# Optimization experiments

Measured on AMD Instinct MI355X. Metric: run time of the kernel, lower is better.

Reference implementation:

```python
import jax, jax.numpy as jnp
import numpy as np

N_LAYERS = 3
NUM_NODES = 400000
EMB_DIM = 64
N_EDGES = 4000000


def setup_inputs() -> dict:
    key = jax.random.key(0)
    k1, k2, k3, k4 = jax.random.split(key, 4)
    embedding = jax.random.normal(k1, (NUM_NODES, EMB_DIM), dtype=jnp.float32) * 0.1
    adj_row = jax.random.randint(k2, (N_EDGES,), 0, NUM_NODES, dtype=jnp.int64)
    adj_col = jax.random.randint(k3, (N_EDGES,), 0, NUM_NODES, dtype=jnp.int64)
    # normalized adjacency values (e.g. 1/sqrt(d_i d_j)); positive, small
    adj_val = jax.random.uniform(k4, (N_EDGES,), dtype=jnp.float32) * 0.01
    return {"embedding": embedding, "adj_row": adj_row, "adj_col": adj_col, "adj_val": adj_val}


def _spmm(row, col, val, x):
    # sparse [N,N] @ dense [N,D]: gather neighbor rows, scale, scatter-add
    msgs = val[:, None] * x[col]                      # [E, D]
    return jax.ops.segment_sum(msgs, row, num_segments=NUM_NODES)


def reference(embedding, adj_row, adj_col, adj_val):
    # LightGCN propagation: running mean over layer outputs (fused accumulator,
    # mathematically identical to stack+mean over n_layers+1 embeddings)
    x = embedding
    acc = x
    for _ in range(N_LAYERS):
        x = _spmm(adj_row, adj_col, adj_val, x)
        acc = acc + x
    all_embeddings = acc / jnp.asarray(N_LAYERS + 1, dtype=x.dtype)
    return all_embeddings
```

## Files before the change

kernel.cpp:

```cpp
#include <hip/hip_runtime.h>

#define EMB 64
#define SCAN_B 256
#define RPB 32
#define RPW 8
#define ECAP 1024

typedef unsigned uint2v __attribute__((ext_vector_type(2)));
typedef float float4v __attribute__((ext_vector_type(4)));

__device__ inline uint2 nt_load_u2(const uint2* p) {
    uint2v v = __builtin_nontemporal_load((const uint2v*)p);
    return make_uint2(v.x, v.y);
}
__device__ inline void nt_store_u2(uint2* p, uint2 v) {
    uint2v t; t.x = v.x; t.y = v.y;
    __builtin_nontemporal_store(t, (uint2v*)p);
}
__device__ inline float4 nt_load_f4(const float4* p) {
    float4v v = __builtin_nontemporal_load((const float4v*)p);
    return make_float4(v.x, v.y, v.z, v.w);
}
__device__ inline void nt_store_f4(float4* p, float4 v) {
    float4v t; t.x = v.x; t.y = v.y; t.z = v.z; t.w = v.w;
    __builtin_nontemporal_store(t, (float4v*)p);
}

__device__ inline unsigned short f2bf(float f) {
    unsigned u = __float_as_uint(f);
    return (unsigned short)((u + 0x7fffu + ((u >> 16) & 1u)) >> 16);
}
__device__ inline float bl(unsigned u) { return __uint_as_float(u << 16); }
__device__ inline float bh(unsigned u) { return __uint_as_float(u & 0xffff0000u); }


__global__ void zero_ints(int* __restrict__ p, int n) {
    int i = blockIdx.x * blockDim.x + threadIdx.x;
    if (i < n) p[i] = 0;
}

__global__ void hist_rows(const int* __restrict__ row, int* __restrict__ S, int E) {
    int e = blockIdx.x * blockDim.x + threadIdx.x;
    if (e < E) atomicAdd(&S[__builtin_nontemporal_load(row + e)], 1);
}

__global__ void scan_block_sums(const int* __restrict__ S, int* __restrict__ bsum, int N) {
    __shared__ int sdata[SCAN_B];
    int i = blockIdx.x * SCAN_B + threadIdx.x;
    sdata[threadIdx.x] = (i < N) ? S[i] : 0;
    __syncthreads();
    for (int off = SCAN_B / 2; off > 0; off >>= 1) {
        if (threadIdx.x < off) sdata[threadIdx.x] += sdata[threadIdx.x + off];
        __syncthreads();
    }
    if (threadIdx.x == 0) bsum[blockIdx.x] = sdata[0];
}

__global__ void scan_sums(int* __restrict__ bsum, int nb) {
    __shared__ int part[1024];
    int t = threadIdx.x;
    int i0 = 2 * t, i1 = 2 * t + 1;
    int a = (i0 < nb) ? bsum[i0] : 0;
    int b = (i1 < nb) ? bsum[i1] : 0;
    part[t] = a + b;
    __syncthreads();
    for (int off = 1; off < 1024; off <<= 1) {
        int v = part[t];
        int add = (t >= off) ? part[t - off] : 0;
        __syncthreads();
        part[t] = v + add;
        __syncthreads();
    }
    int excl = (t == 0) ? 0 : part[t - 1];
    if (i0 < nb) bsum[i0] = excl;
    if (i1 < nb) bsum[i1] = excl + a;
}

__global__ void scan_apply(int* __restrict__ S, const int* __restrict__ bsum, int N) {
    __shared__ int sdata[SCAN_B];
    int i = blockIdx.x * SCAN_B + threadIdx.x;
    int v = (i < N) ? S[i] : 0;
    sdata[threadIdx.x] = v;
    __syncthreads();
    for (int off = 1; off < SCAN_B; off <<= 1) {
        int val = sdata[threadIdx.x];
        int add = (threadIdx.x >= off) ? sdata[threadIdx.x - off] : 0;
        __syncthreads();
        sdata[threadIdx.x] = val + add;
        __syncthreads();
    }
    int excl = (threadIdx.x == 0 ? 0 : sdata[threadIdx.x - 1]) + bsum[blockIdx.x];
    if (i < N) S[i] = excl;
}

__global__ void scatter_edges_ranged(const int* __restrict__ row, const int* __restrict__ col,
                                     const float* __restrict__ val,
                                     int* __restrict__ S, uint2* __restrict__ epack,
                                     int E, int rstep) {
    int pass  = blockIdx.x & 7;
    int chunk = blockIdx.x >> 3;
    int e = chunk * blockDim.x + threadIdx.x;
    if (e >= E) return;
    int r = __builtin_nontemporal_load(row + e);
    int lo = pass * rstep;
    if (r < lo || r >= lo + rstep) return;
    int c = __builtin_nontemporal_load(col + e);
    float v = __builtin_nontemporal_load(val + e);
    int pos = atomicAdd(&S[r], 1);
    epack[pos] = make_uint2((unsigned)c, __float_as_uint(v));
}

__global__ void conv_bf16(const float4* __restrict__ src, uint2* __restrict__ dst, int n4) {
    int i = blockIdx.x * blockDim.x + threadIdx.x;
    if (i < n4) {
        float4 v = nt_load_f4(src + i);
        unsigned w0 = (unsigned)f2bf(v.x) | ((unsigned)f2bf(v.y) << 16);
        unsigned w1 = (unsigned)f2bf(v.z) | ((unsigned)f2bf(v.w) << 16);
        nt_store_u2(dst + i, make_uint2(w0, w1));
    }
}

template<bool STG>
__device__ __forceinline__ void spmm_rows(
    const uint2* __restrict__ epack, const uint2* __restrict__ esh, int beg0,
    const int* __restrict__ Ssh, int j0,
    const unsigned short* __restrict__ x, const float* __restrict__ emb,
    unsigned short* __restrict__ y, float* __restrict__ acc,
    int rb, int N, int mode, int lane, int grp, int d4)
{
    const uint2 z2 = make_uint2(0u, 0u);

#define EDG(i) (STG ? esh[(i) - beg0] : epack[i])
#define LOADR(J, B_, E_, P0, P1, P2, P3, G0, G1, G2, G3)                         \
    {                                                                            \
        B_ = Ssh[J]; E_ = Ssh[(J) + 1];                                          \
        int i0 = B_ + grp, i1 = i0 + 4, i2 = i0 + 8, i3 = i0 + 12;               \
        P0 = (i0 < E_) ? EDG(i0) : z2;                                           \
        P1 = (i1 < E_) ? EDG(i1) : z2;                                           \
        P2 = (i2 < E_) ? EDG(i2) : z2;                                           \
        P3 = (i3 < E_) ? EDG(i3) : z2;                                           \
        G0 = (i0 < E_) ? ((const uint2*)(x + ((size_t)P0.x << 6)))[d4] : z2;     \
        G1 = (i1 < E_) ? ((const uint2*)(x + ((size_t)P1.x << 6)))[d4] : z2;     \
        G2 = (i2 < E_) ? ((const uint2*)(x + ((size_t)P2.x << 6)))[d4] : z2;     \
        G3 = (i3 < E_) ? ((const uint2*)(x + ((size_t)P3.x << 6)))[d4] : z2;     \
    }

    int aB = 0, aE = 0;
    uint2 ap0 = z2, ap1 = z2, ap2 = z2, ap3 = z2, ag0 = z2, ag1 = z2, ag2 = z2, ag3 = z2;
    int bB = 0, bE = 0;
    uint2 bp0 = z2, bp1 = z2, bp2 = z2, bp3 = z2, bg0 = z2, bg1 = z2, bg2 = z2, bg3 = z2;

    LOADR(j0, aB, aE, ap0, ap1, ap2, ap3, ag0, ag1, ag2, ag3);

    for (int k = 0; k < RPW; ++k) {
        int j = j0 + k;
        int r = rb + j;
        if (k + 1 < RPW) {
            LOADR(j + 1, bB, bE, bp0, bp1, bp2, bp3, bg0, bg1, bg2, bg3);
        }

        float4 s = make_float4(0.f, 0.f, 0.f, 0.f);
        {
            int i0 = aB + grp, i1 = i0 + 4, i2 = i0 + 8, i3 = i0 + 12;
            float w0 = (i0 < aE) ? __uint_as_float(ap0.y) : 0.f;
            float w1 = (i1 < aE) ? __uint_as_float(ap1.y) : 0.f;
            float w2 = (i2 < aE) ? __uint_as_float(ap2.y) : 0.f;
            float w3 = (i3 < aE) ? __uint_as_float(ap3.y) : 0.f;
            s.x += w0 * bl(ag0.x); s.y += w0 * bh(ag0.x); s.z += w0 * bl(ag0.y); s.w += w0 * bh(ag0.y);
            s.x += w1 * bl(ag1.x); s.y += w1 * bh(ag1.x); s.z += w1 * bl(ag1.y); s.w += w1 * bh(ag1.y);
            s.x += w2 * bl(ag2.x); s.y += w2 * bh(ag2.x); s.z += w2 * bl(ag2.y); s.w += w2 * bh(ag2.y);
            s.x += w3 * bl(ag3.x); s.y += w3 * bh(ag3.x); s.z += w3 * bl(ag3.y); s.w += w3 * bh(ag3.y);
        }
        for (int base = aB + 16; base < aE; base += 16) {
            int i0 = base + grp, i1 = i0 + 4, i2 = i0 + 8, i3 = i0 + 12;
            uint2 p0 = (i0 < aE) ? EDG(i0) : z2;
            uint2 p1 = (i1 < aE) ? EDG(i1) : z2;
            uint2 p2 = (i2 < aE) ? EDG(i2) : z2;
            uint2 p3 = (i3 < aE) ? EDG(i3) : z2;
            uint2 g0 = (i0 < aE) ? ((const uint2*)(x + ((size_t)p0.x << 6)))[d4] : z2;
            uint2 g1 = (i1 < aE) ? ((const uint2*)(x + ((size_t)p1.x << 6)))[d4] : z2;
            uint2 g2 = (i2 < aE) ? ((const uint2*)(x + ((size_t)p2.x << 6)))[d4] : z2;
            uint2 g3 = (i3 < aE) ? ((const uint2*)(x + ((size_t)p3.x << 6)))[d4] : z2;
            float w0 = (i0 < aE) ? __uint_as_float(p0.y) : 0.f;
            float w1 = (i1 < aE) ? __uint_as_float(p1.y) : 0.f;
            float w2 = (i2 < aE) ? __uint_as_float(p2.y) : 0.f;
            float w3 = (i3 < aE) ? __uint_as_float(p3.y) : 0.f;
            s.x += w0 * bl(g0.x); s.y += w0 * bh(g0.x); s.z += w0 * bl(g0.y); s.w += w0 * bh(g0.y);
            s.x += w1 * bl(g1.x); s.y += w1 * bh(g1.x); s.z += w1 * bl(g1.y); s.w += w1 * bh(g1.y);
            s.x += w2 * bl(g2.x); s.y += w2 * bh(g2.x); s.z += w2 * bl(g2.y); s.w += w2 * bh(g2.y);
            s.x += w3 * bl(g3.x); s.y += w3 * bh(g3.x); s.z += w3 * bl(g3.y); s.w += w3 * bh(g3.y);
        }

        s.x += __shfl_xor(s.x, 32); s.y += __shfl_xor(s.y, 32);
        s.z += __shfl_xor(s.z, 32); s.w += __shfl_xor(s.w, 32);
        s.x += __shfl_xor(s.x, 16); s.y += __shfl_xor(s.y, 16);
        s.z += __shfl_xor(s.z, 16); s.w += __shfl_xor(s.w, 16);

        if (lane < 16 && r < N) {
            size_t o4 = (size_t)r * 16 + d4;
            if (mode != 2) {
                unsigned w0 = (unsigned)f2bf(s.x) | ((unsigned)f2bf(s.y) << 16);
                unsigned w1 = (unsigned)f2bf(s.z) | ((unsigned)f2bf(s.w) << 16);
                nt_store_u2(((uint2*)y) + o4, make_uint2(w0, w1));
            }
            if (mode == 0) {
                float4 e4 = nt_load_f4(((const float4*)emb) + o4);
                nt_store_f4(((float4*)acc) + o4,
                            make_float4(e4.x + s.x, e4.y + s.y, e4.z + s.z, e4.w + s.w));
            } else if (mode == 1) {
                float4 a4 = nt_load_f4(((const float4*)acc) + o4);
                nt_store_f4(((float4*)acc) + o4,
                            make_float4(a4.x + s.x, a4.y + s.y, a4.z + s.z, a4.w + s.w));
            } else if (mode == 2) {
                float4 a4 = nt_load_f4(((const float4*)acc) + o4);
                nt_store_f4(((float4*)acc) + o4,
                            make_float4((a4.x + s.x) * 0.25f, (a4.y + s.y) * 0.25f,
                                        (a4.z + s.z) * 0.25f, (a4.w + s.w) * 0.25f));
            }
        }
        aB = bB; aE = bE;
        ap0 = bp0; ap1 = bp1; ap2 = bp2; ap3 = bp3;
        ag0 = bg0; ag1 = bg1; ag2 = bg2; ag3 = bg3;
    }
#undef LOADR
#undef EDG
}

__global__ __launch_bounds__(256) void spmm_csr2(
    const uint2* __restrict__ epack, const int* __restrict__ S,
    const unsigned short* __restrict__ x, const float* __restrict__ emb,
    unsigned short* __restrict__ y, float* __restrict__ acc,
    int N, int mode)
{
    __shared__ int Ssh[RPB + 1];
    __shared__ uint2 esh[ECAP];

    int tid = threadIdx.x;
    int rb = blockIdx.x * RPB;

    if (tid <= RPB) {
        int rr = rb - 1 + tid;
        Ssh[tid] = (rr < 0) ? 0 : S[rr < N ? rr : (N - 1)];
    }
    __syncthreads();

    int beg0 = Ssh[0];
    int nE = Ssh[RPB] - beg0;
    bool staged = (nE <= ECAP);
    if (staged) {
        for (int i = tid; i < nE; i += 256) esh[i] = nt_load_u2(epack + beg0 + i);
    }
    __syncthreads();

    int wid = tid >> 6, lane = tid & 63;
    int grp = lane >> 4, d4 = lane & 15;
    int j0 = wid * RPW;

    if (staged)
        spmm_rows<true >(epack, esh, beg0, Ssh, j0, x, emb, y, acc, rb, N, mode, lane, grp, d4);
    else
        spmm_rows<false>(epack, esh, beg0, Ssh, j0, x, emb, y, acc, rb, N, mode, lane, grp, d4);
}


__global__ void lgcn_init(const float4* __restrict__ emb, float4* __restrict__ A,
                          float4* __restrict__ acc, float4* __restrict__ B, int n4) {
    int i = blockIdx.x * blockDim.x + threadIdx.x;
    if (i < n4) { float4 v = emb[i]; A[i] = v; acc[i] = v; B[i] = make_float4(0,0,0,0); }
}
__global__ void lgcn_spmm(const int* __restrict__ row, const int* __restrict__ col,
                          const float* __restrict__ val, const float* __restrict__ x,
                          float* __restrict__ y, int E) {
    int gid = blockIdx.x * blockDim.x + threadIdx.x;
    int e = gid >> 6;
    if (e >= E) return;
    int d = threadIdx.x & 63;
    atomicAdd(y + (size_t)row[e] * EMB + d, val[e] * x[(size_t)col[e] * EMB + d]);
}
__global__ void lgcn_addzero(float4* __restrict__ acc, const float4* __restrict__ X,
                             float4* __restrict__ Y, int n4) {
    int i = blockIdx.x * blockDim.x + threadIdx.x;
    if (i < n4) {
        float4 a = acc[i]; float4 xv = X[i];
        a.x += xv.x; a.y += xv.y; a.z += xv.z; a.w += xv.w;
        acc[i] = a; Y[i] = make_float4(0,0,0,0);
    }
}
__global__ void lgcn_final(float4* __restrict__ acc, const float4* __restrict__ X, int n4) {
    int i = blockIdx.x * blockDim.x + threadIdx.x;
    if (i < n4) {
        float4 a = acc[i]; float4 xv = X[i];
        a.x = (a.x + xv.x) * 0.25f; a.y = (a.y + xv.y) * 0.25f;
        a.z = (a.z + xv.z) * 0.25f; a.w = (a.w + xv.w) * 0.25f;
        acc[i] = a;
    }
}

extern "C" void kernel_launch(void* const* d_in, const int* in_sizes, int n_in,
                              void* d_out, int out_size, void* d_ws, size_t ws_size,
                              hipStream_t stream) {
    const float* emb = (const float*)d_in[0];
    const int*   row = (const int*)d_in[1];
    const int*   col = (const int*)d_in[2];
    const float* val = (const float*)d_in[3];
    float* acc = (float*)d_out;

    const int N = in_sizes[0] / EMB;
    const int E = in_sizes[1];
    const int TB = 256;

    const size_t buf_elems = (size_t)N * EMB;
    const int nb = (N + SCAN_B - 1) / SCAN_B;

    const size_t need = (size_t)E * 8 + buf_elems * 2 * 3 + (size_t)N * 4 + (size_t)nb * 4;

    if (ws_size >= need) {
        uint2* epack = (uint2*)d_ws;
        unsigned short* X0 = (unsigned short*)(epack + E);
        unsigned short* X1 = X0 + buf_elems;
        unsigned short* X2 = X1 + buf_elems;
        int* S    = (int*)(X2 + buf_elems);
        int* bsum = S + N;

        const int eb  = (E + TB - 1) / TB;
        const int nbN = (N + TB - 1) / TB;
        const int n4  = (int)(buf_elems / 4);
        const int cvb = (n4 + TB - 1) / TB;
        const int spmm_blocks = (N + RPB - 1) / RPB;
        const int rstep = (N + 7) / 8;

        zero_ints<<<nbN, TB, 0, stream>>>(S, N);
        hist_rows<<<eb, TB, 0, stream>>>(row, S, E);
        scan_block_sums<<<nb, SCAN_B, 0, stream>>>(S, bsum, N);
        scan_sums<<<1, 1024, 0, stream>>>(bsum, nb);
        scan_apply<<<nb, SCAN_B, 0, stream>>>(S, bsum, N);
        scatter_edges_ranged<<<eb * 8, TB, 0, stream>>>(row, col, val, S, epack, E, rstep);
        conv_bf16<<<cvb, TB, 0, stream>>>((const float4*)emb, (uint2*)X0, n4);

        spmm_csr2<<<spmm_blocks, TB, 0, stream>>>(epack, S, X0, emb, X1, acc, N, 0);
        spmm_csr2<<<spmm_blocks, TB, 0, stream>>>(epack, S, X1, nullptr, X2, acc, N, 1);
        spmm_csr2<<<spmm_blocks, TB, 0, stream>>>(epack, S, X2, nullptr, nullptr, acc, N, 2);
    } else {
        float* A = (float*)d_ws;
        float* B = A + buf_elems;
        const int n4 = (int)(buf_elems / 4);
        const int ew_blocks = (n4 + TB - 1) / TB;
        const int spmm_blocks = (E + 3) / 4;
        lgcn_init<<<ew_blocks, TB, 0, stream>>>((const float4*)emb, (float4*)A,
                                                (float4*)acc, (float4*)B, n4);
        lgcn_spmm<<<spmm_blocks, TB, 0, stream>>>(row, col, val, A, B, E);
        lgcn_addzero<<<ew_blocks, TB, 0, stream>>>((float4*)acc, (const float4*)B,
                                                   (float4*)A, n4);
        lgcn_spmm<<<spmm_blocks, TB, 0, stream>>>(row, col, val, B, A, E);
        lgcn_addzero<<<ew_blocks, TB, 0, stream>>>((float4*)acc, (const float4*)A,
                                                   (float4*)B, n4);
        lgcn_spmm<<<spmm_blocks, TB, 0, stream>>>(row, col, val, A, B, E);
        lgcn_final<<<ew_blocks, TB, 0, stream>>>((float4*)acc, (const float4*)B, n4);
    }
}
```

Measured before the change: 1.050 ms.

## Deepen SpMM row prefetch, vectorize histogram, single-pass edge scatter

The SpMM row loop now prefetches two rows ahead instead of one, raises wave priority around the first FMA block, and requests 8 waves per EU through launch bounds. The row histogram reads four row indices per thread with a vector load. The 8-pass range-filtered edge scatter becomes a single pass with nontemporal stores. Together these aim to hide gather latency and cut preprocessing passes over the edge arrays, at the cost of more registers (possible spills under the occupancy bound) and more scattered atomics and writes in the scatter.

```diff
diff --git a/kernel.cpp b/kernel.cpp
--- a/kernel.cpp
+++ b/kernel.cpp
@@ -8,6 +8,7 @@
 
 typedef unsigned uint2v __attribute__((ext_vector_type(2)));
 typedef float float4v __attribute__((ext_vector_type(4)));
+typedef int int4v __attribute__((ext_vector_type(4)));
 
 __device__ inline uint2 nt_load_u2(const uint2* p) {
     uint2v v = __builtin_nontemporal_load((const uint2v*)p);
@@ -42,6 +43,17 @@
 __global__ void hist_rows(const int* __restrict__ row, int* __restrict__ S, int E) {
     int e = blockIdx.x * blockDim.x + threadIdx.x;
     if (e < E) atomicAdd(&S[__builtin_nontemporal_load(row + e)], 1);
+}
+
+__global__ void hist_rows4(const int* __restrict__ row, int* __restrict__ S, int E4) {
+    int i = blockIdx.x * blockDim.x + threadIdx.x;
+    if (i < E4) {
+        int4v r = __builtin_nontemporal_load((const int4v*)row + i);
+        atomicAdd(&S[r.x], 1);
+        atomicAdd(&S[r.y], 1);
+        atomicAdd(&S[r.z], 1);
+        atomicAdd(&S[r.w], 1);
+    }
 }
 
 __global__ void scan_block_sums(const int* __restrict__ S, int* __restrict__ bsum, int N) {
@@ -93,21 +105,16 @@
     if (i < N) S[i] = excl;
 }
 
-__global__ void scatter_edges_ranged(const int* __restrict__ row, const int* __restrict__ col,
-                                     const float* __restrict__ val,
-                                     int* __restrict__ S, uint2* __restrict__ epack,
-                                     int E, int rstep) {
-    int pass  = blockIdx.x & 7;
-    int chunk = blockIdx.x >> 3;
-    int e = chunk * blockDim.x + threadIdx.x;
+__global__ void scatter_edges(const int* __restrict__ row, const int* __restrict__ col,
+                              const float* __restrict__ val,
+                              int* __restrict__ S, uint2* __restrict__ epack, int E) {
+    int e = blockIdx.x * blockDim.x + threadIdx.x;
     if (e >= E) return;
     int r = __builtin_nontemporal_load(row + e);
-    int lo = pass * rstep;
-    if (r < lo || r >= lo + rstep) return;
     int c = __builtin_nontemporal_load(col + e);
     float v = __builtin_nontemporal_load(val + e);
     int pos = atomicAdd(&S[r], 1);
-    epack[pos] = make_uint2((unsigned)c, __float_as_uint(v));
+    nt_store_u2(epack + pos, make_uint2((unsigned)c, __float_as_uint(v)));
 }
 
 __global__ void conv_bf16(const float4* __restrict__ src, uint2* __restrict__ dst, int n4) {
@@ -149,17 +156,21 @@
     uint2 ap0 = z2, ap1 = z2, ap2 = z2, ap3 = z2, ag0 = z2, ag1 = z2, ag2 = z2, ag3 = z2;
     int bB = 0, bE = 0;
     uint2 bp0 = z2, bp1 = z2, bp2 = z2, bp3 = z2, bg0 = z2, bg1 = z2, bg2 = z2, bg3 = z2;
-
-    LOADR(j0, aB, aE, ap0, ap1, ap2, ap3, ag0, ag1, ag2, ag3);
+    int cB = 0, cE = 0;
+    uint2 cp0 = z2, cp1 = z2, cp2 = z2, cp3 = z2, cg0 = z2, cg1 = z2, cg2 = z2, cg3 = z2;
+
+    LOADR(j0,     aB, aE, ap0, ap1, ap2, ap3, ag0, ag1, ag2, ag3);
+    LOADR(j0 + 1, bB, bE, bp0, bp1, bp2, bp3, bg0, bg1, bg2, bg3);
 
     for (int k = 0; k < RPW; ++k) {
         int j = j0 + k;
         int r = rb + j;
-        if (k + 1 < RPW) {
-            LOADR(j + 1, bB, bE, bp0, bp1, bp2, bp3, bg0, bg1, bg2, bg3);
+        if (k + 2 < RPW) {
+            LOADR(j + 2, cB, cE, cp0, cp1, cp2, cp3, cg0, cg1, cg2, cg3);
         }
 
         float4 s = make_float4(0.f, 0.f, 0.f, 0.f);
+        __builtin_amdgcn_s_setprio(1);
         {
             int i0 = aB + grp, i1 = i0 + 4, i2 = i0 + 8, i3 = i0 + 12;
             float w0 = (i0 < aE) ? __uint_as_float(ap0.y) : 0.f;
@@ -171,6 +182,7 @@
             s.x += w2 * bl(ag2.x); s.y += w2 * bh(ag2.x); s.z += w2 * bl(ag2.y); s.w += w2 * bh(ag2.y);
             s.x += w3 * bl(ag3.x); s.y += w3 * bh(ag3.x); s.z += w3 * bl(ag3.y); s.w += w3 * bh(ag3.y);
         }
+        __builtin_amdgcn_s_setprio(0);
         for (int base = aB + 16; base < aE; base += 16) {
             int i0 = base + grp, i1 = i0 + 4, i2 = i0 + 8, i3 = i0 + 12;
             uint2 p0 = (i0 < aE) ? EDG(i0) : z2;
@@ -221,12 +233,15 @@
         aB = bB; aE = bE;
         ap0 = bp0; ap1 = bp1; ap2 = bp2; ap3 = bp3;
         ag0 = bg0; ag1 = bg1; ag2 = bg2; ag3 = bg3;
+        bB = cB; bE = cE;
+        bp0 = cp0; bp1 = cp1; bp2 = cp2; bp3 = cp3;
+        bg0 = cg0; bg1 = cg1; bg2 = cg2; bg3 = cg3;
     }
 #undef LOADR
 #undef EDG
 }
 
-__global__ __launch_bounds__(256) void spmm_csr2(
+__global__ __launch_bounds__(256, 8) void spmm_csr2(
     const uint2* __restrict__ epack, const int* __restrict__ S,
     const unsigned short* __restrict__ x, const float* __restrict__ emb,
     unsigned short* __restrict__ y, float* __restrict__ acc,
@@ -327,14 +342,18 @@
         const int n4  = (int)(buf_elems / 4);
         const int cvb = (n4 + TB - 1) / TB;
         const int spmm_blocks = (N + RPB - 1) / RPB;
-        const int rstep = (N + 7) / 8;
 
         zero_ints<<<nbN, TB, 0, stream>>>(S, N);
-        hist_rows<<<eb, TB, 0, stream>>>(row, S, E);
+        if ((E & 3) == 0) {
+            const int e4b = (E / 4 + TB - 1) / TB;
+            hist_rows4<<<e4b, TB, 0, stream>>>(row, S, E / 4);
+        } else {
+            hist_rows<<<eb, TB, 0, stream>>>(row, S, E);
+        }
         scan_block_sums<<<nb, SCAN_B, 0, stream>>>(S, bsum, N);
         scan_sums<<<1, 1024, 0, stream>>>(bsum, nb);
         scan_apply<<<nb, SCAN_B, 0, stream>>>(S, bsum, N);
-        scatter_edges_ranged<<<eb * 8, TB, 0, stream>>>(row, col, val, S, epack, E, rstep);
+        scatter_edges<<<eb, TB, 0, stream>>>(row, col, val, S, epack, E);
         conv_bf16<<<cvb, TB, 0, stream>>>((const float4*)emb, (uint2*)X0, n4);
 
         spmm_csr2<<<spmm_blocks, TB, 0, stream>>>(epack, S, X0, emb, X1, acc, N, 0);
```

After: 1.359 ms. +29.4%, slower.
